# Kernel optimization log

Measured on AMD Instinct MI355X. Metric: run time of the kernel, lower is better.

## Reference

```python
import jax, jax.numpy as jnp
import numpy as np

N_STEPS = 8          # spatial_interval
SPATIAL_SCALE = 1.0  # spatial_scale


def setup_inputs() -> dict:
    key = jax.random.key(0)
    ks = jax.random.split(key, 6)
    B, N, D = 32, 1024, 256
    x = jax.random.normal(ks[0], (B, N, D), dtype=jnp.float32)
    adj_mx = jax.random.uniform(ks[1], (N, N), dtype=jnp.float32) / N  # row-scaled dense adjacency
    alpha_train = jnp.ones((N,), dtype=jnp.float32)          # alpha * ones(num_node), alpha=1.0
    w = jnp.eye(D, dtype=jnp.float32) + 0.01 * jax.random.normal(ks[2], (D, D), dtype=jnp.float32)
    d = jax.random.uniform(ks[3], (D,), dtype=jnp.float32)
    fc_in_w = jax.random.normal(ks[4], (D, D), dtype=jnp.float32) * (1.0 / np.sqrt(D))
    fc_in_b = jnp.zeros((D,), dtype=jnp.float32)
    return {"x": x, "adj_mx": adj_mx, "alpha_train": alpha_train, "w": w,
            "d": d, "fc_in_w": fc_in_w, "fc_in_b": fc_in_b, "vt": 0}


def reference(x, adj_mx, alpha_train, w, d, fc_in_w, fc_in_b, vt):
    # x: [B, N, D]. x0 is detached in torch (x.clone().detach()).
    x0 = jax.lax.stop_gradient(x)
    # fc_in (dropout is identity in eval mode)
    h = jnp.einsum('bnd,ed->bne', x, fc_in_w) + fc_in_b
    # constants of the diffusion ODE
    alph = jax.nn.sigmoid(alpha_train)[:, None]          # [N, 1]
    d_clamped = jnp.clip(d, 0.0, 1.0)
    w_eff = (w * d_clamped) @ w.T                        # [D, D]
    dt = jnp.float32(SPATIAL_SCALE / N_STEPS)

    def euler_step(h, _):
        ax = jnp.einsum('nm,bmd->bnd', adj_mx, h)        # graph diffusion
        f = alph * 0.5 * (ax - h) + h @ w_eff - h + x0
        return h + dt * f, None

    h, _ = jax.lax.scan(euler_step, h, None, length=N_STEPS)
    return h
```

## Files before the change

### kernel.cpp

```cpp
#include <hip/hip_runtime.h>
#include <hip/hip_bf16.h>
#include <stdint.h>

typedef __bf16 bf16;
typedef __bf16 bf16x8 __attribute__((ext_vector_type(8)));
typedef __bf16 bf16x4 __attribute__((ext_vector_type(4)));
typedef float f32x4 __attribute__((ext_vector_type(4)));


__device__ __forceinline__ void gload_lds16(const bf16* g, bf16* l) {
    __builtin_amdgcn_global_load_lds(
        (const __attribute__((address_space(1))) void*)g,
        (__attribute__((address_space(3))) void*)l, 16, 0, 0);
}

__device__ __forceinline__ void stageA(const bf16* __restrict__ g, int lda,
                                       bf16* l, int t) {
#pragma unroll
    for (int i = 0; i < 4; ++i) {
        int c = (i << 8) + t;
        int row = c >> 3, slot = c & 7;
        gload_lds16(g + (size_t)row * lda + ((slot ^ (row & 7)) << 3), l + c * 8);
    }
}
__device__ __forceinline__ void stageB(const bf16* __restrict__ g, int ldb,
                                       bf16* l, int t) {
#pragma unroll
    for (int i = 0; i < 2; ++i) {
        int c = (i << 8) + t;
        int row = c >> 3, slot = c & 7;
        gload_lds16(g + (size_t)row * ldb + ((slot ^ (row & 7)) << 3), l + c * 8);
    }
}

__device__ __forceinline__ void mma_tile(const bf16* A, const bf16* B,
                                         f32x4 acc[2][4], int lane, int wv) {
    const int r0 = wv * 32 + (lane & 15);
    const int kq = lane >> 4;
    bf16x8 a[2][2], b[4][2];
#pragma unroll
    for (int mi = 0; mi < 2; ++mi) {
        int rA = r0 + mi * 16;
#pragma unroll
        for (int kk = 0; kk < 2; ++kk) {
            int kc = kk * 4 + kq;
            a[mi][kk] = *(const bf16x8*)&A[rA * 64 + ((kc ^ (rA & 7)) << 3)];
        }
    }
#pragma unroll
    for (int ni = 0; ni < 4; ++ni) {
        int rB = ni * 16 + (lane & 15);
#pragma unroll
        for (int kk = 0; kk < 2; ++kk) {
            int kc = kk * 4 + kq;
            b[ni][kk] = *(const bf16x8*)&B[rB * 64 + ((kc ^ (rB & 7)) << 3)];
        }
    }
#pragma unroll
    for (int kk = 0; kk < 2; ++kk)
#pragma unroll
        for (int mi = 0; mi < 2; ++mi)
#pragma unroll
            for (int ni = 0; ni < 4; ++ni)
                acc[mi][ni] = __builtin_amdgcn_mfma_f32_16x16x32_bf16(
                    a[mi][kk], b[ni][kk], acc[mi][ni], 0, 0, 0);
}

template <int NT, typename F>
__device__ __forceinline__ void run_pipeline(F tadr, bf16 (*As)[8192],
                                             bf16 (*Bs)[4096], f32x4 acc[2][4],
                                             int t, int lane, int wv) {
    {
        const bf16 *Ag, *Bg; int lda, ldb;
        tadr(0, Ag, lda, Bg, ldb);
        stageA(Ag, lda, As[0], t);
        stageB(Bg, ldb, Bs[0], t);
        if (NT > 1) {
            tadr(1, Ag, lda, Bg, ldb);
            stageA(Ag, lda, As[1], t);
            stageB(Bg, ldb, Bs[1], t);
        }
    }
    int cur = 0, pre = 2;
#pragma unroll 1
    for (int i = 0; i < NT; ++i) {
        if (i + 2 < NT) {
            const bf16 *Ag, *Bg; int lda, ldb;
            tadr(i + 2, Ag, lda, Bg, ldb);
            stageA(Ag, lda, As[pre], t);
            stageB(Bg, ldb, Bs[pre], t);
            asm volatile("s_waitcnt vmcnt(12)" ::: "memory");
        } else if (i + 1 < NT) {
            asm volatile("s_waitcnt vmcnt(6)" ::: "memory");
        } else {
            asm volatile("s_waitcnt vmcnt(0)" ::: "memory");
        }
        __builtin_amdgcn_s_barrier();
        __builtin_amdgcn_s_setprio(1);
        mma_tile(As[cur], Bs[cur], acc, lane, wv);
        __builtin_amdgcn_s_setprio(0);
        __builtin_amdgcn_s_barrier();
        cur = (cur == 2) ? 0 : cur + 1;
        pre = (pre == 2) ? 0 : pre + 1;
    }
}

__global__ void prep_alpha(const float* __restrict__ a, float* __restrict__ out) {
    int i = blockIdx.x * blockDim.x + threadIdx.x;
    if (i < 1024) out[i] = 0.5f / (1.0f + __expf(-a[i]));
}

__global__ void prep_adj(const float* __restrict__ adj, const float* __restrict__ ahs,
                         bf16* __restrict__ adjb) {
    int i = blockIdx.x * blockDim.x + threadIdx.x;
    int row = i >> 8;
    float s = ahs[row];
    float4 v = ((const float4*)adj)[i];
    bf16x4 o = {(bf16)(s * v.x), (bf16)(s * v.y), (bf16)(s * v.z), (bf16)(s * v.w)};
    ((bf16x4*)adjb)[i] = o;
}

__global__ void cast_f32_bf16x4(const float* __restrict__ src, bf16* __restrict__ dst,
                                int n4) {
    int i = blockIdx.x * blockDim.x + threadIdx.x;
    if (i < n4) {
        float4 v = ((const float4*)src)[i];
        bf16x4 o = {(bf16)v.x, (bf16)v.y, (bf16)v.z, (bf16)v.w};
        ((bf16x4*)dst)[i] = o;
    }
}

__global__ void prep_weff(const float* __restrict__ w, const float* __restrict__ dv,
                          bf16* __restrict__ weffT) {
    __shared__ float wk[256];
    __shared__ float dd[256];
    int k = blockIdx.x, j = threadIdx.x;
    dd[j] = fminf(fmaxf(dv[j], 0.0f), 1.0f);
    wk[j] = w[k * 256 + j];
    __syncthreads();
    float s = 0.0f;
#pragma unroll 8
    for (int c = 0; c < 256; ++c) s += wk[c] * dd[c] * w[j * 256 + c];
    weffT[j * 256 + k] = (bf16)s;
}

__launch_bounds__(256, 2)
__global__ void gemm_fcin(const bf16* __restrict__ xb, const bf16* __restrict__ fcwb,
                          const float* __restrict__ fcb,
                          bf16* __restrict__ hb, bf16* __restrict__ hT,
                          bf16* __restrict__ hlo) {
    __shared__ __align__(16) bf16 As[3][8192];
    __shared__ __align__(16) bf16 Bs[3][4096];
    int t = threadIdx.x, lane = t & 63, wv = t >> 6;
    int row0 = blockIdx.y * 128;
    int col0 = blockIdx.x * 64;
    f32x4 acc[2][4] = {};
    const bf16* Ab = xb + (size_t)row0 * 256;
    const bf16* Bb = fcwb + (size_t)col0 * 256;
    auto tadr = [&](int i, const bf16*& Ag, int& lda, const bf16*& Bg, int& ldb) {
        Ag = Ab + i * 64; lda = 256;
        Bg = Bb + i * 64; ldb = 256;
    };
    run_pipeline<4>(tadr, As, Bs, acc, t, lane, wv);

    int rbase = row0 + wv * 32 + ((lane >> 4) << 2);
    int cbase = col0 + (lane & 15);
#pragma unroll
    for (int mi = 0; mi < 2; ++mi) {
        int rg = rbase + mi * 16;
#pragma unroll
        for (int ni = 0; ni < 4; ++ni) {
            int col = cbase + ni * 16;
            float bias = fcb[col];
            bf16x4 tv;
#pragma unroll
            for (int r = 0; r < 4; ++r) {
                float v = acc[mi][ni][r] + bias;
                size_t idx = (size_t)(rg + r) * 256 + col;
                bf16 hi = (bf16)v;
                bf16 lo = (bf16)(v - (float)hi);
                hb[idx] = hi;
                hlo[idx] = lo;
                tv[r] = hi;
            }
            int b = rg >> 10, n = rg & 1023;
            *(bf16x4*)&hT[(((size_t)(b * 256 + col)) << 10) + n] = tv;
        }
    }
}

template <bool LAST>
__launch_bounds__(256, 2)
__global__ void gemm_step(const bf16* __restrict__ adjb, const bf16* __restrict__ hbp,
                          const bf16* __restrict__ hTp, const bf16* __restrict__ weffT,
                          const float* __restrict__ ahs, const bf16* __restrict__ x0b,
                          bf16* __restrict__ hlo, bf16* __restrict__ hbn,
                          bf16* __restrict__ hTn, float* __restrict__ out) {
    __shared__ __align__(16) bf16 As[3][8192];
    __shared__ __align__(16) bf16 Bs[3][4096];
    int t = threadIdx.x, lane = t & 63, wv = t >> 6;
    int g = blockIdx.x;
    int xcd = g & 7, rest = g >> 3;
    int xy = rest & 31;
    int b = (rest >> 5) * 8 + xcd;
    int d0 = (xy & 3) * 64;
    int n0 = (xy >> 2) * 128;
    f32x4 acc[2][4] = {};

    const bf16* A1 = adjb + (size_t)n0 * 1024;
    const bf16* B1 = hTp + ((size_t)(b * 256 + d0)) * 1024;
    const bf16* A2 = hbp + ((size_t)(b * 1024 + n0)) * 256;
    const bf16* B2 = weffT + (size_t)d0 * 256;
    auto tadr = [&](int i, const bf16*& Ag, int& lda, const bf16*& Bg, int& ldb) {
        if (i < 16) {
            Ag = A1 + i * 64; lda = 1024;
            Bg = B1 + i * 64; ldb = 1024;
        } else {
            Ag = A2 + (i - 16) * 64; lda = 256;
            Bg = B2 + (i - 16) * 64; ldb = 256;
        }
    };
    run_pipeline<20>(tadr, As, Bs, acc, t, lane, wv);

    const float dt = 0.125f;
    int rb = wv * 32 + ((lane >> 4) << 2);
    int cb = d0 + (lane & 15);
#pragma unroll
    for (int mi = 0; mi < 2; ++mi) {
        int nr = n0 + rb + mi * 16;
#pragma unroll
        for (int ni = 0; ni < 4; ++ni) {
            int col = cb + ni * 16;
            bf16x4 tv;
#pragma unroll
            for (int r = 0; r < 4; ++r) {
                int node = nr + r;
                size_t idx = (((size_t)b << 10) + node) * 256 + col;
                float hi = (float)hbp[idx];
                float lo = (float)hlo[idx];
                float hold = hi + lo;
                float x0v = (float)x0b[idx];
                float f = acc[mi][ni][r] - (ahs[node] + 1.0f) * hold + x0v;
                float hv = hold + dt * f;
                if (LAST) {
                    out[idx] = hv;
                } else {
                    bf16 nhi = (bf16)hv;
                    bf16 nlo = (bf16)(hv - (float)nhi);
                    hbn[idx] = nhi;
                    hlo[idx] = nlo;
                    tv[r] = nhi;
                }
            }
            if (!LAST)
                *(bf16x4*)&hTn[(((size_t)(b * 256 + col)) << 10) + nr] = tv;
        }
    }
}

extern "C" void kernel_launch(void* const* d_in, const int* in_sizes, int n_in,
                              void* d_out, int out_size, void* d_ws, size_t ws_size,
                              hipStream_t stream) {
    const float* x     = (const float*)d_in[0];
    const float* adj   = (const float*)d_in[1];
    const float* alpha = (const float*)d_in[2];
    const float* w     = (const float*)d_in[3];
    const float* dvec  = (const float*)d_in[4];
    const float* fcw   = (const float*)d_in[5];
    const float* fcb   = (const float*)d_in[6];
    float* out = (float*)d_out;

    const size_t HB = (size_t)32 * 1024 * 256 * 2;
    char* p = (char*)d_ws;
    bf16* hb0   = (bf16*)p; p += HB;
    bf16* hb1   = (bf16*)p; p += HB;
    bf16* hT0   = (bf16*)p; p += HB;
    bf16* hT1   = (bf16*)p; p += HB;
    bf16* xb    = (bf16*)p; p += HB;
    bf16* hlo   = (bf16*)p; p += HB;
    bf16* adjb  = (bf16*)p; p += (size_t)1024 * 1024 * 2;
    bf16* fcwb  = (bf16*)p; p += 256 * 256 * 2;
    bf16* weffT = (bf16*)p; p += 256 * 256 * 2;
    float* ahs  = (float*)p; p += 1024 * 4;

    prep_alpha<<<4, 256, 0, stream>>>(alpha, ahs);
    prep_adj<<<1024, 256, 0, stream>>>(adj, ahs, adjb);
    prep_weff<<<256, 256, 0, stream>>>(w, dvec, weffT);
    cast_f32_bf16x4<<<8192, 256, 0, stream>>>(x, xb, 2097152);
    cast_f32_bf16x4<<<64, 256, 0, stream>>>(fcw, fcwb, 16384);

    gemm_fcin<<<dim3(4, 256), 256, 0, stream>>>(xb, fcwb, fcb, hb0, hT0, hlo);

    bf16* hb[2] = {hb0, hb1};
    bf16* hT[2] = {hT0, hT1};
    int cur = 0;
    for (int s = 0; s < 8; ++s) {
        if (s < 7)
            gemm_step<false><<<1024, 256, 0, stream>>>(
                adjb, hb[cur], hT[cur], weffT, ahs, xb, hlo,
                hb[cur ^ 1], hT[cur ^ 1], out);
        else
            gemm_step<true><<<1024, 256, 0, stream>>>(
                adjb, hb[cur], hT[cur], weffT, ahs, xb, hlo,
                hb[cur ^ 1], hT[cur ^ 1], out);
        cur ^= 1;
    }
}
```

Measured before the change: 450.9 us.

## Enlarge step GEMM tile to 256x128 with 8 waves and 4x4 MFMA per wave

The per-step fused GEMM moves from 128x64 tiles with 4 waves (1024 blocks) to 256x128 tiles with 8 waves in a 4x2 grid (256 blocks). Each wave now computes a 64x64 sub-tile, and a new triple-buffered pipeline with explicit vmcnt waits and setprio stages twice as much data per k-step. The goal is more operand reuse per LDS load and less global traffic for the adjacency and h tiles. The cost is 144KB of LDS, one block per CU, only 256 blocks for 256 CUs, and higher register pressure.

```diff
diff --git a/kernel.cpp b/kernel.cpp
--- a/kernel.cpp
+++ b/kernel.cpp
@@ -7,11 +7,85 @@
 typedef __bf16 bf16x4 __attribute__((ext_vector_type(4)));
 typedef float f32x4 __attribute__((ext_vector_type(4)));
 
-
 __device__ __forceinline__ void gload_lds16(const bf16* g, bf16* l) {
     __builtin_amdgcn_global_load_lds(
         (const __attribute__((address_space(1))) void*)g,
         (__attribute__((address_space(3))) void*)l, 16, 0, 0);
+}
+
+template <int ROWS>
+__device__ __forceinline__ void stageRows(const bf16* __restrict__ g, int ld,
+                                          bf16* l, int t) {
+#pragma unroll
+    for (int i = 0; i < ROWS * 8 / 512; ++i) {
+        int c = i * 512 + t;
+        int row = c >> 3, slot = c & 7;
+        gload_lds16(g + (size_t)row * ld + ((slot ^ (row & 7)) << 3), l + c * 8);
+    }
+}
+
+__device__ __forceinline__ void mma_fat(const bf16* A, const bf16* B,
+                                        f32x4 acc[4][4], int lane, int wm, int wn) {
+    const int l15 = lane & 15;
+    const int kq = lane >> 4;
+#pragma unroll
+    for (int kk = 0; kk < 2; ++kk) {
+        int kc = kk * 4 + kq;
+        bf16x8 a[4], b[4];
+#pragma unroll
+        for (int mi = 0; mi < 4; ++mi) {
+            int rA = wm * 64 + mi * 16 + l15;
+            a[mi] = *(const bf16x8*)&A[rA * 64 + ((kc ^ (rA & 7)) << 3)];
+        }
+#pragma unroll
+        for (int ni = 0; ni < 4; ++ni) {
+            int rB = wn * 64 + ni * 16 + l15;
+            b[ni] = *(const bf16x8*)&B[rB * 64 + ((kc ^ (rB & 7)) << 3)];
+        }
+#pragma unroll
+        for (int mi = 0; mi < 4; ++mi)
+#pragma unroll
+            for (int ni = 0; ni < 4; ++ni)
+                acc[mi][ni] = __builtin_amdgcn_mfma_f32_16x16x32_bf16(
+                    a[mi], b[ni], acc[mi][ni], 0, 0, 0);
+    }
+}
+
+template <int NT, typename F>
+__device__ __forceinline__ void run_pipe2(F tadr, bf16 (*As)[16384], bf16 (*Bs)[8192],
+                                          f32x4 acc[4][4], int t, int lane,
+                                          int wm, int wn) {
+    {
+        const bf16 *Ag, *Bg; int lda, ldb;
+        tadr(0, Ag, lda, Bg, ldb);
+        stageRows<256>(Ag, lda, As[0], t);
+        stageRows<128>(Bg, ldb, Bs[0], t);
+        tadr(1, Ag, lda, Bg, ldb);
+        stageRows<256>(Ag, lda, As[1], t);
+        stageRows<128>(Bg, ldb, Bs[1], t);
+    }
+    int cur = 0, pre = 2;
+#pragma unroll 1
+    for (int i = 0; i < NT; ++i) {
+        if (i + 2 < NT) {
+            const bf16 *Ag, *Bg; int lda, ldb;
+            tadr(i + 2, Ag, lda, Bg, ldb);
+            stageRows<256>(Ag, lda, As[pre], t);
+            stageRows<128>(Bg, ldb, Bs[pre], t);
+            asm volatile("s_waitcnt vmcnt(12)" ::: "memory");
+        } else if (i + 1 < NT) {
+            asm volatile("s_waitcnt vmcnt(6)" ::: "memory");
+        } else {
+            asm volatile("s_waitcnt vmcnt(0)" ::: "memory");
+        }
+        __builtin_amdgcn_s_barrier();
+        __builtin_amdgcn_s_setprio(1);
+        mma_fat(As[cur], Bs[cur], acc, lane, wm, wn);
+        __builtin_amdgcn_s_setprio(0);
+        __builtin_amdgcn_s_barrier();
+        cur = (cur == 2) ? 0 : cur + 1;
+        pre = (pre == 2) ? 0 : pre + 1;
+    }
 }
 
 __device__ __forceinline__ void stageA(const bf16* __restrict__ g, int lda,
@@ -190,22 +264,23 @@
 }
 
 template <bool LAST>
-__launch_bounds__(256, 2)
+__launch_bounds__(512, 1)
 __global__ void gemm_step(const bf16* __restrict__ adjb, const bf16* __restrict__ hbp,
                           const bf16* __restrict__ hTp, const bf16* __restrict__ weffT,
                           const float* __restrict__ ahs, const bf16* __restrict__ x0b,
                           bf16* __restrict__ hlo, bf16* __restrict__ hbn,
                           bf16* __restrict__ hTn, float* __restrict__ out) {
-    __shared__ __align__(16) bf16 As[3][8192];
-    __shared__ __align__(16) bf16 Bs[3][4096];
+    __shared__ __align__(16) bf16 As[3][16384];
+    __shared__ __align__(16) bf16 Bs[3][8192];
     int t = threadIdx.x, lane = t & 63, wv = t >> 6;
+    int wm = wv >> 1, wn = wv & 1;
     int g = blockIdx.x;
-    int xcd = g & 7, rest = g >> 3;
-    int xy = rest & 31;
-    int b = (rest >> 5) * 8 + xcd;
-    int d0 = (xy & 3) * 64;
-    int n0 = (xy >> 2) * 128;
-    f32x4 acc[2][4] = {};
+    int xcd = g & 7, idx = g >> 3;
+    int b = (idx & 3) * 8 + xcd;
+    int tile = idx >> 2;
+    int n0 = (tile & 3) * 256;
+    int d0 = (tile >> 2) * 128;
+    f32x4 acc[4][4] = {};
 
     const bf16* A1 = adjb + (size_t)n0 * 1024;
     const bf16* B1 = hTp + ((size_t)(b * 256 + d0)) * 1024;
@@ -220,35 +295,34 @@
             Bg = B2 + (i - 16) * 64; ldb = 256;
         }
     };
-    run_pipeline<20>(tadr, As, Bs, acc, t, lane, wv);
+    run_pipe2<20>(tadr, As, Bs, acc, t, lane, wm, wn);
 
     const float dt = 0.125f;
-    int rb = wv * 32 + ((lane >> 4) << 2);
-    int cb = d0 + (lane & 15);
-#pragma unroll
-    for (int mi = 0; mi < 2; ++mi) {
-        int nr = n0 + rb + mi * 16;
+    int l15 = lane & 15;
+    int lq = (lane >> 4) << 2;
+#pragma unroll
+    for (int mi = 0; mi < 4; ++mi) {
+        int nr = n0 + wm * 64 + mi * 16 + lq;
 #pragma unroll
         for (int ni = 0; ni < 4; ++ni) {
-            int col = cb + ni * 16;
+            int col = d0 + wn * 64 + ni * 16 + l15;
             bf16x4 tv;
 #pragma unroll
             for (int r = 0; r < 4; ++r) {
                 int node = nr + r;
-                size_t idx = (((size_t)b << 10) + node) * 256 + col;
-                float hi = (float)hbp[idx];
-                float lo = (float)hlo[idx];
+                size_t idx2 = (((size_t)b << 10) + node) * 256 + col;
+                float hi = (float)hbp[idx2];
+                float lo = (float)hlo[idx2];
                 float hold = hi + lo;
-                float x0v = (float)x0b[idx];
-                float f = acc[mi][ni][r] - (ahs[node] + 1.0f) * hold + x0v;
+                float f = acc[mi][ni][r] - (ahs[node] + 1.0f) * hold + (float)x0b[idx2];
                 float hv = hold + dt * f;
                 if (LAST) {
-                    out[idx] = hv;
+                    out[idx2] = hv;
                 } else {
                     bf16 nhi = (bf16)hv;
                     bf16 nlo = (bf16)(hv - (float)nhi);
-                    hbn[idx] = nhi;
-                    hlo[idx] = nlo;
+                    hbn[idx2] = nhi;
+                    hlo[idx2] = nlo;
                     tv[r] = nhi;
                 }
             }
@@ -296,11 +370,11 @@
     int cur = 0;
     for (int s = 0; s < 8; ++s) {
         if (s < 7)
-            gemm_step<false><<<1024, 256, 0, stream>>>(
+            gemm_step<false><<<256, 512, 0, stream>>>(
                 adjb, hb[cur], hT[cur], weffT, ahs, xb, hlo,
                 hb[cur ^ 1], hT[cur ^ 1], out);
         else
-            gemm_step<true><<<1024, 256, 0, stream>>>(
+            gemm_step<true><<<256, 512, 0, stream>>>(
                 adjb, hb[cur], hT[cur], weffT, ahs, xb, hlo,
                 hb[cur ^ 1], hT[cur ^ 1], out);
         cur ^= 1;
```

After: 432.3 us. 4.1% less time.

## Enlarge step GEMM tiles to 256x128 with 8 waves and transposed epilogue

Applied to the files above, without the earlier changes.

Each Euler step GEMM now uses 256x128 output tiles computed by 512-thread blocks (8 waves, 64x64 per wave) with a hand-interleaved 3-stage LDS pipeline. Global-to-LDS loads are split across the MFMA phases. The epilogue reads old h, its low part and x0 in the transposed layout, so loads are contiguous bf16x4. The row-major next h is written through an LDS transpose image using 16-byte stores. The goal is more data reuse per block and less uncoalesced epilogue traffic. In exchange, occupancy drops to one block of 144KB LDS per CU and only 256 blocks are launched.

```diff
diff --git a/kernel.cpp b/kernel.cpp
--- a/kernel.cpp
+++ b/kernel.cpp
@@ -6,7 +6,7 @@
 typedef __bf16 bf16x8 __attribute__((ext_vector_type(8)));
 typedef __bf16 bf16x4 __attribute__((ext_vector_type(4)));
 typedef float f32x4 __attribute__((ext_vector_type(4)));
-
+typedef unsigned short u16;
 
 __device__ __forceinline__ void gload_lds16(const bf16* g, bf16* l) {
     __builtin_amdgcn_global_load_lds(
@@ -14,23 +14,110 @@
         (__attribute__((address_space(3))) void*)l, 16, 0, 0);
 }
 
+__device__ __forceinline__ void stChunk(const bf16* __restrict__ g, int ld,
+                                        bf16* l, int c) {
+    int row = c >> 3, slot = c & 7;
+    gload_lds16(g + (size_t)row * ld + ((slot ^ (row & 7)) << 3), l + c * 8);
+}
+
+__device__ __forceinline__ void mma8(const bf16x8& a0, const bf16x8& a1,
+                                     const bf16x8& b0, const bf16x8& b1,
+                                     const bf16x8& b2, const bf16x8& b3,
+                                     f32x4 (&acc)[4][4], int mi) {
+    acc[mi][0] = __builtin_amdgcn_mfma_f32_16x16x32_bf16(a0, b0, acc[mi][0], 0, 0, 0);
+    acc[mi][1] = __builtin_amdgcn_mfma_f32_16x16x32_bf16(a0, b1, acc[mi][1], 0, 0, 0);
+    acc[mi][2] = __builtin_amdgcn_mfma_f32_16x16x32_bf16(a0, b2, acc[mi][2], 0, 0, 0);
+    acc[mi][3] = __builtin_amdgcn_mfma_f32_16x16x32_bf16(a0, b3, acc[mi][3], 0, 0, 0);
+    acc[mi+1][0] = __builtin_amdgcn_mfma_f32_16x16x32_bf16(a1, b0, acc[mi+1][0], 0, 0, 0);
+    acc[mi+1][1] = __builtin_amdgcn_mfma_f32_16x16x32_bf16(a1, b1, acc[mi+1][1], 0, 0, 0);
+    acc[mi+1][2] = __builtin_amdgcn_mfma_f32_16x16x32_bf16(a1, b2, acc[mi+1][2], 0, 0, 0);
+    acc[mi+1][3] = __builtin_amdgcn_mfma_f32_16x16x32_bf16(a1, b3, acc[mi+1][3], 0, 0, 0);
+}
+
+#define PHASE_SYNC_PRE()                                        \
+    __builtin_amdgcn_s_barrier();                               \
+    asm volatile("s_waitcnt lgkmcnt(0)" ::: "memory");          \
+    __builtin_amdgcn_sched_barrier(0);                          \
+    __builtin_amdgcn_s_setprio(1);
+#define PHASE_SYNC_POST()                                       \
+    __builtin_amdgcn_s_setprio(0);                              \
+    __builtin_amdgcn_s_barrier();
+
+__global__ void prep_alpha(const float* __restrict__ a, float* __restrict__ out) {
+    int i = blockIdx.x * blockDim.x + threadIdx.x;
+    if (i < 1024) out[i] = 0.5f / (1.0f + __expf(-a[i]));
+}
+
+__global__ void prep_adj(const float* __restrict__ adj, const float* __restrict__ ahs,
+                         bf16* __restrict__ adjb) {
+    int i = blockIdx.x * blockDim.x + threadIdx.x;
+    int row = i >> 8;
+    float s = ahs[row];
+    float4 v = ((const float4*)adj)[i];
+    bf16x4 o = {(bf16)(s * v.x), (bf16)(s * v.y), (bf16)(s * v.z), (bf16)(s * v.w)};
+    ((bf16x4*)adjb)[i] = o;
+}
+
+__global__ void cast_f32_bf16x4(const float* __restrict__ src, bf16* __restrict__ dst,
+                                int n4) {
+    int i = blockIdx.x * blockDim.x + threadIdx.x;
+    if (i < n4) {
+        float4 v = ((const float4*)src)[i];
+        bf16x4 o = {(bf16)v.x, (bf16)v.y, (bf16)v.z, (bf16)v.w};
+        ((bf16x4*)dst)[i] = o;
+    }
+}
+
+__global__ void prep_weff(const float* __restrict__ w, const float* __restrict__ dv,
+                          bf16* __restrict__ weffT) {
+    __shared__ float wk[256];
+    __shared__ float dd[256];
+    int k = blockIdx.x, j = threadIdx.x;
+    dd[j] = fminf(fmaxf(dv[j], 0.0f), 1.0f);
+    wk[j] = w[k * 256 + j];
+    __syncthreads();
+    float s = 0.0f;
+#pragma unroll 8
+    for (int c = 0; c < 256; ++c) s += wk[c] * dd[c] * w[j * 256 + c];
+    weffT[j * 256 + k] = (bf16)s;
+}
+
+__global__ void prep_xT(const float* __restrict__ x, bf16* __restrict__ xT,
+                        bf16* __restrict__ xb) {
+    __shared__ bf16 tile[64][65];
+    int b = blockIdx.z, n0 = blockIdx.x * 64, d0 = blockIdx.y * 64;
+    int t = threadIdx.x;
+    int i = t >> 4, j4 = (t & 15) * 4;
+#pragma unroll
+    for (int p = 0; p < 4; ++p) {
+        int n = i + p * 16;
+        size_t gi = (((size_t)b << 10) + n0 + n) * 256 + d0 + j4;
+        float4 v = *(const float4*)&x[gi];
+        bf16x4 o = {(bf16)v.x, (bf16)v.y, (bf16)v.z, (bf16)v.w};
+        *(bf16x4*)&xb[gi] = o;
+        tile[n][j4 + 0] = o[0]; tile[n][j4 + 1] = o[1];
+        tile[n][j4 + 2] = o[2]; tile[n][j4 + 3] = o[3];
+    }
+    __syncthreads();
+#pragma unroll
+    for (int p = 0; p < 4; ++p) {
+        int c = p * 256 + t;
+        int d = c >> 4, nc = c & 15;
+        bf16x4 o = {tile[nc * 4 + 0][d], tile[nc * 4 + 1][d],
+                    tile[nc * 4 + 2][d], tile[nc * 4 + 3][d]};
+        *(bf16x4*)&xT[(((size_t)(b * 256 + d0 + d)) << 10) + n0 + nc * 4] = o;
+    }
+}
+
 __device__ __forceinline__ void stageA(const bf16* __restrict__ g, int lda,
                                        bf16* l, int t) {
 #pragma unroll
-    for (int i = 0; i < 4; ++i) {
-        int c = (i << 8) + t;
-        int row = c >> 3, slot = c & 7;
-        gload_lds16(g + (size_t)row * lda + ((slot ^ (row & 7)) << 3), l + c * 8);
-    }
+    for (int i = 0; i < 4; ++i) stChunk(g, lda, l, (i << 8) + t);
 }
 __device__ __forceinline__ void stageB(const bf16* __restrict__ g, int ldb,
                                        bf16* l, int t) {
 #pragma unroll
-    for (int i = 0; i < 2; ++i) {
-        int c = (i << 8) + t;
-        int row = c >> 3, slot = c & 7;
-        gload_lds16(g + (size_t)row * ldb + ((slot ^ (row & 7)) << 3), l + c * 8);
-    }
+    for (int i = 0; i < 2; ++i) stChunk(g, ldb, l, (i << 8) + t);
 }
 
 __device__ __forceinline__ void mma_tile(const bf16* A, const bf16* B,
@@ -105,50 +192,11 @@
     }
 }
 
-__global__ void prep_alpha(const float* __restrict__ a, float* __restrict__ out) {
-    int i = blockIdx.x * blockDim.x + threadIdx.x;
-    if (i < 1024) out[i] = 0.5f / (1.0f + __expf(-a[i]));
-}
-
-__global__ void prep_adj(const float* __restrict__ adj, const float* __restrict__ ahs,
-                         bf16* __restrict__ adjb) {
-    int i = blockIdx.x * blockDim.x + threadIdx.x;
-    int row = i >> 8;
-    float s = ahs[row];
-    float4 v = ((const float4*)adj)[i];
-    bf16x4 o = {(bf16)(s * v.x), (bf16)(s * v.y), (bf16)(s * v.z), (bf16)(s * v.w)};
-    ((bf16x4*)adjb)[i] = o;
-}
-
-__global__ void cast_f32_bf16x4(const float* __restrict__ src, bf16* __restrict__ dst,
-                                int n4) {
-    int i = blockIdx.x * blockDim.x + threadIdx.x;
-    if (i < n4) {
-        float4 v = ((const float4*)src)[i];
-        bf16x4 o = {(bf16)v.x, (bf16)v.y, (bf16)v.z, (bf16)v.w};
-        ((bf16x4*)dst)[i] = o;
-    }
-}
-
-__global__ void prep_weff(const float* __restrict__ w, const float* __restrict__ dv,
-                          bf16* __restrict__ weffT) {
-    __shared__ float wk[256];
-    __shared__ float dd[256];
-    int k = blockIdx.x, j = threadIdx.x;
-    dd[j] = fminf(fmaxf(dv[j], 0.0f), 1.0f);
-    wk[j] = w[k * 256 + j];
-    __syncthreads();
-    float s = 0.0f;
-#pragma unroll 8
-    for (int c = 0; c < 256; ++c) s += wk[c] * dd[c] * w[j * 256 + c];
-    weffT[j * 256 + k] = (bf16)s;
-}
-
 __launch_bounds__(256, 2)
 __global__ void gemm_fcin(const bf16* __restrict__ xb, const bf16* __restrict__ fcwb,
                           const float* __restrict__ fcb,
                           bf16* __restrict__ hb, bf16* __restrict__ hT,
-                          bf16* __restrict__ hlo) {
+                          bf16* __restrict__ hloT) {
     __shared__ __align__(16) bf16 As[3][8192];
     __shared__ __align__(16) bf16 Bs[3][4096];
     int t = threadIdx.x, lane = t & 63, wv = t >> 6;
@@ -172,88 +220,182 @@
         for (int ni = 0; ni < 4; ++ni) {
             int col = cbase + ni * 16;
             float bias = fcb[col];
-            bf16x4 tv;
+            bf16x4 tv, lv;
 #pragma unroll
             for (int r = 0; r < 4; ++r) {
                 float v = acc[mi][ni][r] + bias;
                 size_t idx = (size_t)(rg + r) * 256 + col;
                 bf16 hi = (bf16)v;
-                bf16 lo = (bf16)(v - (float)hi);
                 hb[idx] = hi;
-                hlo[idx] = lo;
                 tv[r] = hi;
+                lv[r] = (bf16)(v - (float)hi);
             }
             int b = rg >> 10, n = rg & 1023;
-            *(bf16x4*)&hT[(((size_t)(b * 256 + col)) << 10) + n] = tv;
+            size_t tb = (((size_t)(b * 256 + col)) << 10) + n;
+            *(bf16x4*)&hT[tb] = tv;
+            *(bf16x4*)&hloT[tb] = lv;
         }
     }
 }
 
 template <bool LAST>
-__launch_bounds__(256, 2)
+__launch_bounds__(512, 1)
 __global__ void gemm_step(const bf16* __restrict__ adjb, const bf16* __restrict__ hbp,
                           const bf16* __restrict__ hTp, const bf16* __restrict__ weffT,
-                          const float* __restrict__ ahs, const bf16* __restrict__ x0b,
-                          bf16* __restrict__ hlo, bf16* __restrict__ hbn,
+                          const float* __restrict__ ahs, const bf16* __restrict__ xT,
+                          bf16* __restrict__ hloT, bf16* __restrict__ hbn,
                           bf16* __restrict__ hTn, float* __restrict__ out) {
-    __shared__ __align__(16) bf16 As[3][8192];
-    __shared__ __align__(16) bf16 Bs[3][4096];
+    __shared__ __align__(16) char smem[147456];
+    bf16 (*As)[16384] = (bf16(*)[16384])smem;
+    bf16 (*Bs)[8192]  = (bf16(*)[8192])(smem + 98304);
     int t = threadIdx.x, lane = t & 63, wv = t >> 6;
+    int wm = wv >> 1, wn = wv & 1;
     int g = blockIdx.x;
-    int xcd = g & 7, rest = g >> 3;
-    int xy = rest & 31;
-    int b = (rest >> 5) * 8 + xcd;
-    int d0 = (xy & 3) * 64;
-    int n0 = (xy >> 2) * 128;
-    f32x4 acc[2][4] = {};
+    int xcd = g & 7, bidx = g >> 3;
+    int b = (bidx & 3) * 8 + xcd;
+    int tile = bidx >> 2;
+    int n0 = (tile & 3) * 256;
+    int d0 = (tile >> 2) * 128;
+    f32x4 acc[4][4] = {};
 
     const bf16* A1 = adjb + (size_t)n0 * 1024;
     const bf16* B1 = hTp + ((size_t)(b * 256 + d0)) * 1024;
     const bf16* A2 = hbp + ((size_t)(b * 1024 + n0)) * 256;
     const bf16* B2 = weffT + (size_t)d0 * 256;
-    auto tadr = [&](int i, const bf16*& Ag, int& lda, const bf16*& Bg, int& ldb) {
-        if (i < 16) {
-            Ag = A1 + i * 64; lda = 1024;
-            Bg = B1 + i * 64; ldb = 1024;
-        } else {
-            Ag = A2 + (i - 16) * 64; lda = 256;
-            Bg = B2 + (i - 16) * 64; ldb = 256;
-        }
+    auto tadr = [&](int i, const bf16*& Ag, int& la, const bf16*& Bg, int& lb) {
+        if (i < 16) { Ag = A1 + i * 64; la = 1024; Bg = B1 + i * 64; lb = 1024; }
+        else        { Ag = A2 + (i - 16) * 64; la = 256; Bg = B2 + (i - 16) * 64; lb = 256; }
     };
-    run_pipeline<20>(tadr, As, Bs, acc, t, lane, wv);
+    const int NT = 20;
+    {
+        const bf16 *Ag, *Bg; int la, lb;
+        tadr(0, Ag, la, Bg, lb);
+#pragma unroll
+        for (int k = 0; k < 4; ++k) stChunk(Ag, la, As[0], k * 512 + t);
+#pragma unroll
+        for (int k = 0; k < 2; ++k) stChunk(Bg, lb, Bs[0], k * 512 + t);
+        tadr(1, Ag, la, Bg, lb);
+#pragma unroll
+        for (int k = 0; k < 4; ++k) stChunk(Ag, la, As[1], k * 512 + t);
+#pragma unroll
+        for (int k = 0; k < 2; ++k) stChunk(Bg, lb, Bs[1], k * 512 + t);
+    }
+    asm volatile("s_waitcnt vmcnt(6)" ::: "memory");
+    __builtin_amdgcn_s_barrier();
+
+    const int l15 = lane & 15, kq = lane >> 4;
+    const int rA0 = wm * 64 + l15, rB0 = wn * 64 + l15;
+    int cur = 0;
+#pragma unroll 1
+    for (int i = 0; i < NT; ++i) {
+        const bf16* A = As[cur];
+        const bf16* B = Bs[cur];
+        int pre = cur + 2; if (pre >= 3) pre -= 3;
+        const bf16 *Ag = nullptr, *Bg = nullptr; int la = 0, lb = 0;
+        const bool st = (i + 2 < NT);
+        if (st) tadr(i + 2, Ag, la, Bg, lb);
+
+        bf16x8 a0, a1, b0, b1, b2, b3;
+        {
+            int kc = kq;
+            b0 = *(const bf16x8*)&B[(rB0     ) * 64 + ((kc ^ ((rB0     ) & 7)) << 3)];
+            b1 = *(const bf16x8*)&B[(rB0 + 16) * 64 + ((kc ^ ((rB0 + 16) & 7)) << 3)];
+            b2 = *(const bf16x8*)&B[(rB0 + 32) * 64 + ((kc ^ ((rB0 + 32) & 7)) << 3)];
+            b3 = *(const bf16x8*)&B[(rB0 + 48) * 64 + ((kc ^ ((rB0 + 48) & 7)) << 3)];
+            a0 = *(const bf16x8*)&A[(rA0     ) * 64 + ((kc ^ ((rA0     ) & 7)) << 3)];
+            a1 = *(const bf16x8*)&A[(rA0 + 16) * 64 + ((kc ^ ((rA0 + 16) & 7)) << 3)];
+            if (st) { stChunk(Ag, la, As[pre], t); stChunk(Ag, la, As[pre], 512 + t); }
+            PHASE_SYNC_PRE(); mma8(a0, a1, b0, b1, b2, b3, acc, 0); PHASE_SYNC_POST();
+        }
+        {
+            int kc = kq;
+            a0 = *(const bf16x8*)&A[(rA0 + 32) * 64 + ((kc ^ ((rA0 + 32) & 7)) << 3)];
+            a1 = *(const bf16x8*)&A[(rA0 + 48) * 64 + ((kc ^ ((rA0 + 48) & 7)) << 3)];
+            if (st) { stChunk(Ag, la, As[pre], 1024 + t); stChunk(Ag, la, As[pre], 1536 + t); }
+            PHASE_SYNC_PRE(); mma8(a0, a1, b0, b1, b2, b3, acc, 2); PHASE_SYNC_POST();
+        }
+        {
+            int kc = 4 + kq;
+            b0 = *(const bf16x8*)&B[(rB0     ) * 64 + ((kc ^ ((rB0     ) & 7)) << 3)];
+            b1 = *(const bf16x8*)&B[(rB0 + 16) * 64 + ((kc ^ ((rB0 + 16) & 7)) << 3)];
+            b2 = *(const bf16x8*)&B[(rB0 + 32) * 64 + ((kc ^ ((rB0 + 32) & 7)) << 3)];
+            b3 = *(const bf16x8*)&B[(rB0 + 48) * 64 + ((kc ^ ((rB0 + 48) & 7)) << 3)];
+            a0 = *(const bf16x8*)&A[(rA0     ) * 64 + ((kc ^ ((rA0     ) & 7)) << 3)];
+            a1 = *(const bf16x8*)&A[(rA0 + 16) * 64 + ((kc ^ ((rA0 + 16) & 7)) << 3)];
+            if (st) { stChunk(Bg, lb, Bs[pre], t); stChunk(Bg, lb, Bs[pre], 512 + t); }
+            PHASE_SYNC_PRE(); mma8(a0, a1, b0, b1, b2, b3, acc, 0); PHASE_SYNC_POST();
+        }
+        {
+            int kc = 4 + kq;
+            a0 = *(const bf16x8*)&A[(rA0 + 32) * 64 + ((kc ^ ((rA0 + 32) & 7)) << 3)];
+            a1 = *(const bf16x8*)&A[(rA0 + 48) * 64 + ((kc ^ ((rA0 + 48) & 7)) << 3)];
+            if (st) asm volatile("s_waitcnt vmcnt(6)" ::: "memory");
+            else    asm volatile("s_waitcnt vmcnt(0)" ::: "memory");
+            PHASE_SYNC_PRE(); mma8(a0, a1, b0, b1, b2, b3, acc, 2); PHASE_SYNC_POST();
+        }
+        cur = cur + 1; if (cur == 3) cur = 0;
+    }
 
     const float dt = 0.125f;
-    int rb = wv * 32 + ((lane >> 4) << 2);
-    int cb = d0 + (lane & 15);
-#pragma unroll
-    for (int mi = 0; mi < 2; ++mi) {
-        int nr = n0 + rb + mi * 16;
+    const int lq = (lane >> 4) << 2;
+    bf16* img = (bf16*)smem;
+    const int PADN = 260;
+#pragma unroll
+    for (int mi = 0; mi < 4; ++mi) {
+        int nl = wm * 64 + mi * 16 + lq;
+        int ng = n0 + nl;
+        f32x4 av = *(const f32x4*)&ahs[ng];
 #pragma unroll
         for (int ni = 0; ni < 4; ++ni) {
-            int col = cb + ni * 16;
-            bf16x4 tv;
+            int cl = wn * 64 + ni * 16 + l15;
+            int cg = d0 + cl;
+            size_t tb = (((size_t)(b * 256 + cg)) << 10) + ng;
+            bf16x4 hp = *(const bf16x4*)&hTp[tb];
+            bf16x4 lp = *(const bf16x4*)&hloT[tb];
+            bf16x4 xp = *(const bf16x4*)&xT[tb];
+            bf16x4 nhi, nlo;
 #pragma unroll
             for (int r = 0; r < 4; ++r) {
-                int node = nr + r;
-                size_t idx = (((size_t)b << 10) + node) * 256 + col;
-                float hi = (float)hbp[idx];
-                float lo = (float)hlo[idx];
-                float hold = hi + lo;
-                float x0v = (float)x0b[idx];
-                float f = acc[mi][ni][r] - (ahs[node] + 1.0f) * hold + x0v;
+                float hold = (float)hp[r] + (float)lp[r];
+                float f = acc[mi][ni][r] - (av[r] + 1.0f) * hold + (float)xp[r];
                 float hv = hold + dt * f;
                 if (LAST) {
-                    out[idx] = hv;
+                    out[(((size_t)b << 10) + ng + r) * 256 + cg] = hv;
                 } else {
-                    bf16 nhi = (bf16)hv;
-                    bf16 nlo = (bf16)(hv - (float)nhi);
-                    hbn[idx] = nhi;
-                    hlo[idx] = nlo;
-                    tv[r] = nhi;
+                    bf16 hi2 = (bf16)hv;
+                    nhi[r] = hi2;
+                    nlo[r] = (bf16)(hv - (float)hi2);
                 }
             }
-            if (!LAST)
-                *(bf16x4*)&hTn[(((size_t)(b * 256 + col)) << 10) + nr] = tv;
+            if (!LAST) {
+                *(bf16x4*)&hTn[tb] = nhi;
+                *(bf16x4*)&hloT[tb] = nlo;
+                int nsw = nl ^ (((cl >> 3) & 7) << 2);
+                *(bf16x4*)&img[cl * PADN + nsw] = nhi;
+            }
+        }
+    }
+    if (!LAST) {
+        asm volatile("s_waitcnt lgkmcnt(0)" ::: "memory");
+        __builtin_amdgcn_s_barrier();
+        const u16* imgu = (const u16*)img;
+#pragma unroll
+        for (int P = 0; P < 8; ++P) {
+            int chunk = P * 512 + t;
+            int node = chunk >> 4;
+            int c8 = chunk & 15;
+            u16 v[8];
+#pragma unroll
+            for (int k = 0; k < 8; ++k) {
+                int col = c8 * 8 + k;
+                v[k] = imgu[col * PADN + (node ^ (((col >> 3) & 7) << 2))];
+            }
+            uint4 pk;
+            pk.x = v[0] | ((unsigned)v[1] << 16);
+            pk.y = v[2] | ((unsigned)v[3] << 16);
+            pk.z = v[4] | ((unsigned)v[5] << 16);
+            pk.w = v[6] | ((unsigned)v[7] << 16);
+            *(uint4*)&hbn[(((size_t)b << 10) + n0 + node) * 256 + d0 + c8 * 8] = pk;
         }
     }
 }
@@ -277,7 +419,8 @@
     bf16* hT0   = (bf16*)p; p += HB;
     bf16* hT1   = (bf16*)p; p += HB;
     bf16* xb    = (bf16*)p; p += HB;
-    bf16* hlo   = (bf16*)p; p += HB;
+    bf16* hloT  = (bf16*)p; p += HB;
+    bf16* xT    = (bf16*)p; p += HB;
     bf16* adjb  = (bf16*)p; p += (size_t)1024 * 1024 * 2;
     bf16* fcwb  = (bf16*)p; p += 256 * 256 * 2;
     bf16* weffT = (bf16*)p; p += 256 * 256 * 2;
@@ -286,22 +429,22 @@
     prep_alpha<<<4, 256, 0, stream>>>(alpha, ahs);
     prep_adj<<<1024, 256, 0, stream>>>(adj, ahs, adjb);
     prep_weff<<<256, 256, 0, stream>>>(w, dvec, weffT);
-    cast_f32_bf16x4<<<8192, 256, 0, stream>>>(x, xb, 2097152);
+    prep_xT<<<dim3(16, 4, 32), 256, 0, stream>>>(x, xT, xb);
     cast_f32_bf16x4<<<64, 256, 0, stream>>>(fcw, fcwb, 16384);
 
-    gemm_fcin<<<dim3(4, 256), 256, 0, stream>>>(xb, fcwb, fcb, hb0, hT0, hlo);
+    gemm_fcin<<<dim3(4, 256), 256, 0, stream>>>(xb, fcwb, fcb, hb0, hT0, hloT);
 
     bf16* hb[2] = {hb0, hb1};
     bf16* hT[2] = {hT0, hT1};
     int cur = 0;
     for (int s = 0; s < 8; ++s) {
         if (s < 7)
-            gemm_step<false><<<1024, 256, 0, stream>>>(
-                adjb, hb[cur], hT[cur], weffT, ahs, xb, hlo,
+            gemm_step<false><<<256, 512, 0, stream>>>(
+                adjb, hb[cur], hT[cur], weffT, ahs, xT, hloT,
                 hb[cur ^ 1], hT[cur ^ 1], out);
         else
-            gemm_step<true><<<1024, 256, 0, stream>>>(
-                adjb, hb[cur], hT[cur], weffT, ahs, xb, hlo,
+            gemm_step<true><<<256, 512, 0, stream>>>(
+                adjb, hb[cur], hT[cur], weffT, ahs, xT, hloT,
                 hb[cur ^ 1], hT[cur ^ 1], out);
         cur ^= 1;
     }
```

Result: faster. 404.9 us (-10.2%).
